# Performance work log

Measured on AMD Instinct MI355X. Metric: run time of the kernel, lower is better.

Reference implementation:

```python
import jax, jax.numpy as jnp
import numpy as np

N, E, IN, H, OUT, K = 50000, 800000, 128, 64, 64, 1024


def setup_inputs() -> dict:
    key = jax.random.key(0)
    ks = jax.random.split(key, 8)
    x = jax.random.normal(ks[0], (N, IN), dtype=jnp.float32)
    edge_index = jax.random.randint(ks[1], (2, E), 0, N, dtype=jnp.int32)
    cluster_id = jax.random.randint(ks[2], (N,), 0, K, dtype=jnp.int32)
    W1 = jax.random.normal(ks[3], (IN, H), dtype=jnp.float32) / np.float32(np.sqrt(IN))
    b1 = jnp.zeros((H,), jnp.float32)
    W2 = jax.random.normal(ks[4], (H, OUT), dtype=jnp.float32) / np.float32(np.sqrt(H))
    b2 = jnp.zeros((OUT,), jnp.float32)
    W_skip = jax.random.normal(ks[5], (H, OUT), dtype=jnp.float32) / np.float32(np.sqrt(H))
    b_skip = jnp.zeros((OUT,), jnp.float32)
    alpha = jnp.full((1,), 1.5, jnp.float32)
    return dict(x=x, edge_index=edge_index, cluster_id=cluster_id, W1=W1, b1=b1,
                W2=W2, b2=b2, W_skip=W_skip, b_skip=b_skip, alpha=alpha)


def gcn_conv_sparse(x, src, dst, n, W, b):
    # PyG GCNConv: transform, then D^{-1/2}(A+I)D^{-1/2} aggregation, then bias.
    h = x @ W  # [n, F_out]
    deg = jax.ops.segment_sum(jnp.ones_like(src, dtype=h.dtype), dst, num_segments=n) + 1.0
    dinv = jax.lax.rsqrt(deg)
    norm = dinv[src] * dinv[dst]  # [E]
    agg = jax.ops.segment_sum(h[src] * norm[:, None], dst, num_segments=n)
    agg = agg + (dinv * dinv)[:, None] * h  # self-loop term
    return agg + b


def reference(x, edge_index, cluster_id, W1, b1, W2, b2, W_skip, b_skip, alpha):
    src, dst = edge_index[0], edge_index[1]
    # conv1 + ReLU (dropout is identity in eval mode)
    x1 = jax.nn.relu(gcn_conv_sparse(x, src, dst, N, W1, b1))  # [N, H]

    # pool_by_partition: scatter-mean node features into K clusters
    sums = jax.ops.segment_sum(x1, cluster_id, num_segments=K)  # [K, H]
    counts = jnp.maximum(jax.ops.segment_sum(jnp.ones((N,), x1.dtype), cluster_id, num_segments=K), 1.0)
    x_p = sums / counts[:, None]

    # deduped pooled edges, self-loops removed == dense 0/1 adjacency with zero diag (K small)
    cu, cv = cluster_id[src], cluster_id[dst]
    A = jnp.zeros((K, K), x1.dtype).at[cu, cv].set(1.0)
    A = A * (1.0 - jnp.eye(K, dtype=x1.dtype))
    A_hat = A + jnp.eye(K, dtype=x1.dtype)
    deg_p = jnp.sum(A_hat, axis=0)  # in-degree at target (PyG computes deg on col)
    dinv_p = jax.lax.rsqrt(deg_p)
    A_norm = dinv_p[:, None] * A_hat * dinv_p[None, :]  # [src, dst]
    h_p = x_p @ W2
    x_p2 = jnp.einsum('st,sf->tf', A_norm, h_p) + b2  # [K, OUT]

    # gather-broadcast + strengthened skip head
    up = x_p2[cluster_id]  # [N, OUT]
    skip = x1 @ W_skip + b_skip
    logits = up + jax.nn.relu(alpha)[0] * skip
    return logits
```

## Files before the change

kernel.cpp:

```cpp
#include <hip/hip_runtime.h>
#include <hip/hip_fp16.h>

#define NN 50000
#define NE 800000
#define FIN 128
#define FH 64
#define FOUT 64
#define KC 1024
#define CAP 64
#define EPB 2048
#define NCH ((NE + EPB - 1) / EPB)
#define NBK ((NN + 255) / 256)
#define BCAP 4608

typedef unsigned char  u8;
typedef unsigned short u16;
typedef unsigned int   u32;

__global__ __launch_bounds__(256) void k_part(const int* __restrict__ src,
                                              const int* __restrict__ dst,
                                              const int* __restrict__ cid,
                                              int* __restrict__ gcur,
                                              u32* __restrict__ bin,
                                              u8* __restrict__ AT) {
    __shared__ int hist[256], off[256], cur[256], gbase[256];
    __shared__ u32 raw[EPB];
    __shared__ u32 sorted[EPB];
    int t = threadIdx.x;
    hist[t] = 0; cur[t] = 0;
    __syncthreads();
    int e0 = blockIdx.x * EPB, e1 = min(NE, e0 + EPB);
    int cnt = e1 - e0;
    for (int e = e0 + t; e < e1; e += 256) {
        int d = dst[e], s = src[e];
        int b = d >> 8, local = d & 255;
        int cu = cid[s], cv = cid[d];
        if (cu != cv) AT[(size_t)cv * KC + cu] = 1;
        atomicAdd(&hist[b], 1);
        raw[e - e0] = ((u32)b << 24) | ((u32)local << 16) | (u32)s;
    }
    __syncthreads();
    int v = hist[t];
    off[t] = v;
    __syncthreads();
    for (int o = 1; o < 256; o <<= 1) {
        int u = (t >= o) ? off[t - o] : 0;
        __syncthreads();
        off[t] += u;
        __syncthreads();
    }
    int ex = off[t] - v;
    __syncthreads();
    off[t] = ex;
    __syncthreads();
    for (int i = t; i < cnt; i += 256) {
        u32 e = raw[i];
        int b = e >> 24;
        int p = off[b] + atomicAdd(&cur[b], 1);
        sorted[p] = e;
    }
    __syncthreads();
    if (t < NBK && hist[t]) gbase[t] = atomicAdd(&gcur[t], hist[t]);
    __syncthreads();
    for (int i = t; i < cnt; i += 256) {
        u32 e = sorted[i];
        int b = e >> 24;
        int idx = gbase[b] + (i - off[b]);
        if (idx < BCAP) bin[(size_t)b * BCAP + idx] = e;
    }
}

__global__ __launch_bounds__(256) void k_slots(const int* __restrict__ gcur,
                                               const u32* __restrict__ bin,
                                               const int* __restrict__ cid,
                                               int* __restrict__ deg,
                                               float* __restrict__ dinv,
                                               int* __restrict__ counts,
                                               u16* __restrict__ slots) {
    __shared__ u16 sbuf[256 * CAP];
    __shared__ int c_lds[256];
    int t = threadIdx.x, b = blockIdx.x;
    c_lds[t] = 0;
    __syncthreads();
    int cnt = min(gcur[b], BCAP);
    const u32* bp = bin + (size_t)b * BCAP;
    for (int i = t; i < cnt; i += 256) {
        u32 e = bp[i];
        int local = (e >> 16) & 255;
        int pos = atomicAdd(&c_lds[local], 1);
        if (pos < CAP) sbuf[local * CAP + pos] = (u16)(e & 0xffffu);
    }
    __syncthreads();
    int node = b * 256 + t;
    if (node < NN) {
        int d = c_lds[t];
        deg[node] = d;
        dinv[node] = rsqrtf((float)d + 1.0f);
        atomicAdd(&counts[cid[node]], 1);
    }
    int rows = min(256, NN - b * 256);
    int n4 = rows * (CAP * 2 / 16);
    const uint4* sb4 = (const uint4*)sbuf;
    uint4* gs4 = (uint4*)(slots + (size_t)b * 256 * CAP);
    for (int j = t; j < n4; j += 256) gs4[j] = sb4[j];
}

__global__ __launch_bounds__(256) void k_gemm1(const float* __restrict__ x,
                                               const float* __restrict__ W1,
                                               const float* __restrict__ dinv,
                                               __half* __restrict__ h) {
    __shared__ float Ws[FIN * FH];
    __shared__ float Xs[32 * FIN];
    int t = threadIdx.x;
    int row_base = blockIdx.x * 32;
    for (int i = t; i < FIN * FH; i += 256) Ws[i] = W1[i];
    {
        const float4* x4 = (const float4*)x;
        float4* xs4 = (float4*)Xs;
        for (int i = t; i < 32 * 32; i += 256) {
            int r = i >> 5, k4 = i & 31;
            int row = row_base + r;
            float4 v = make_float4(0.f, 0.f, 0.f, 0.f);
            if (row < NN) v = x4[(size_t)row * 32 + k4];
            xs4[i] = v;
        }
    }
    __syncthreads();
    int c = t & 31, grp = t >> 5;
    int colp = c * 2;
    int r0 = grp * 4;
    const float4* p0 = (const float4*)&Xs[(r0 + 0) * FIN];
    const float4* p1 = (const float4*)&Xs[(r0 + 1) * FIN];
    const float4* p2 = (const float4*)&Xs[(r0 + 2) * FIN];
    const float4* p3 = (const float4*)&Xs[(r0 + 3) * FIN];
    float acc00 = 0.f, acc01 = 0.f, acc10 = 0.f, acc11 = 0.f;
    float acc20 = 0.f, acc21 = 0.f, acc30 = 0.f, acc31 = 0.f;
#pragma unroll 2
    for (int k4 = 0; k4 < FIN / 4; ++k4) {
        float4 a0 = p0[k4], a1 = p1[k4], a2 = p2[k4], a3 = p3[k4];
        const float* wb = &Ws[(k4 * 4) * FH + colp];
        float2 w0 = *(const float2*)&wb[0];
        float2 w1 = *(const float2*)&wb[FH];
        float2 w2 = *(const float2*)&wb[2 * FH];
        float2 w3 = *(const float2*)&wb[3 * FH];
        acc00 = fmaf(a0.x, w0.x, fmaf(a0.y, w1.x, fmaf(a0.z, w2.x, fmaf(a0.w, w3.x, acc00))));
        acc01 = fmaf(a0.x, w0.y, fmaf(a0.y, w1.y, fmaf(a0.z, w2.y, fmaf(a0.w, w3.y, acc01))));
        acc10 = fmaf(a1.x, w0.x, fmaf(a1.y, w1.x, fmaf(a1.z, w2.x, fmaf(a1.w, w3.x, acc10))));
        acc11 = fmaf(a1.x, w0.y, fmaf(a1.y, w1.y, fmaf(a1.z, w2.y, fmaf(a1.w, w3.y, acc11))));
        acc20 = fmaf(a2.x, w0.x, fmaf(a2.y, w1.x, fmaf(a2.z, w2.x, fmaf(a2.w, w3.x, acc20))));
        acc21 = fmaf(a2.x, w0.y, fmaf(a2.y, w1.y, fmaf(a2.z, w2.y, fmaf(a2.w, w3.y, acc21))));
        acc30 = fmaf(a3.x, w0.x, fmaf(a3.y, w1.x, fmaf(a3.z, w2.x, fmaf(a3.w, w3.x, acc30))));
        acc31 = fmaf(a3.x, w0.y, fmaf(a3.y, w1.y, fmaf(a3.z, w2.y, fmaf(a3.w, w3.y, acc31))));
    }
    __half2* h2 = (__half2*)h;
    int row0 = row_base + r0;
    if (row0 + 0 < NN) { float di = dinv[row0 + 0]; h2[(size_t)(row0 + 0) * 32 + c] = __floats2half2_rn(di * acc00, di * acc01); }
    if (row0 + 1 < NN) { float di = dinv[row0 + 1]; h2[(size_t)(row0 + 1) * 32 + c] = __floats2half2_rn(di * acc10, di * acc11); }
    if (row0 + 2 < NN) { float di = dinv[row0 + 2]; h2[(size_t)(row0 + 2) * 32 + c] = __floats2half2_rn(di * acc20, di * acc21); }
    if (row0 + 3 < NN) { float di = dinv[row0 + 3]; h2[(size_t)(row0 + 3) * 32 + c] = __floats2half2_rn(di * acc30, di * acc31); }
}

__global__ __launch_bounds__(256) void k_gather(const int* __restrict__ deg,
                                                const u16* __restrict__ slots,
                                                const float* __restrict__ dinv,
                                                const __half* __restrict__ h,
                                                const float* __restrict__ b1,
                                                const int* __restrict__ cid,
                                                __half* __restrict__ x1,
                                                float* __restrict__ sums) {
    int lane = threadIdx.x & 63;
    int node = blockIdx.x * 4 + (threadIdx.x >> 6);
    if (node >= NN) return;
    int g = lane >> 3, w = lane & 7;
    const uint4* h16 = (const uint4*)h;
    int cnt = min(deg[node], CAP);
    const u16* cp = slots + (size_t)node * CAP;
    float a0 = 0.f, a1 = 0.f, a2 = 0.f, a3 = 0.f;
    float a4 = 0.f, a5 = 0.f, a6 = 0.f, a7 = 0.f;
    int s = (lane < cnt) ? (int)cp[lane] : 0;
    int nFull = cnt >> 3;
    for (int j = 0; j < nFull; ++j) {
        int ss = __shfl(s, j * 8 + g);
        uint4 u = h16[(size_t)ss * 8 + w];
        float2 f0 = __half22float2(*(__half2*)&u.x);
        float2 f1 = __half22float2(*(__half2*)&u.y);
        float2 f2 = __half22float2(*(__half2*)&u.z);
        float2 f3 = __half22float2(*(__half2*)&u.w);
        a0 += f0.x; a1 += f0.y; a2 += f1.x; a3 += f1.y;
        a4 += f2.x; a5 += f2.y; a6 += f3.x; a7 += f3.y;
    }
    int tail = cnt & 7;
    if (tail) {
        int ss = __shfl(s, nFull * 8 + g);
        float m = (g < tail) ? 1.f : 0.f;
        uint4 u = h16[(size_t)ss * 8 + w];
        float2 f0 = __half22float2(*(__half2*)&u.x);
        float2 f1 = __half22float2(*(__half2*)&u.y);
        float2 f2 = __half22float2(*(__half2*)&u.z);
        float2 f3 = __half22float2(*(__half2*)&u.w);
        a0 = fmaf(m, f0.x, a0); a1 = fmaf(m, f0.y, a1);
        a2 = fmaf(m, f1.x, a2); a3 = fmaf(m, f1.y, a3);
        a4 = fmaf(m, f2.x, a4); a5 = fmaf(m, f2.y, a5);
        a6 = fmaf(m, f3.x, a6); a7 = fmaf(m, f3.y, a7);
    }
#pragma unroll
    for (int msk = 8; msk <= 32; msk <<= 1) {
        a0 += __shfl_xor(a0, msk); a1 += __shfl_xor(a1, msk);
        a2 += __shfl_xor(a2, msk); a3 += __shfl_xor(a3, msk);
        a4 += __shfl_xor(a4, msk); a5 += __shfl_xor(a5, msk);
        a6 += __shfl_xor(a6, msk); a7 += __shfl_xor(a7, msk);
    }
    float di = dinv[node];
    uint4 su = h16[(size_t)node * 8 + w];
    float2 s0 = __half22float2(*(__half2*)&su.x);
    float2 s1 = __half22float2(*(__half2*)&su.y);
    float2 s2 = __half22float2(*(__half2*)&su.z);
    float2 s3 = __half22float2(*(__half2*)&su.w);
    const float4* b14 = (const float4*)b1;
    float4 bA = b14[w * 2], bB = b14[w * 2 + 1];
    float v0 = fmaxf(fmaf(di, a0 + s0.x, bA.x), 0.f);
    float v1 = fmaxf(fmaf(di, a1 + s0.y, bA.y), 0.f);
    float v2 = fmaxf(fmaf(di, a2 + s1.x, bA.z), 0.f);
    float v3 = fmaxf(fmaf(di, a3 + s1.y, bA.w), 0.f);
    float v4 = fmaxf(fmaf(di, a4 + s2.x, bB.x), 0.f);
    float v5 = fmaxf(fmaf(di, a5 + s2.y, bB.y), 0.f);
    float v6 = fmaxf(fmaf(di, a6 + s3.x, bB.z), 0.f);
    float v7 = fmaxf(fmaf(di, a7 + s3.y, bB.w), 0.f);
    if (g == 0) {
        __half2 q0 = __floats2half2_rn(v0, v1);
        __half2 q1 = __floats2half2_rn(v2, v3);
        __half2 q2 = __floats2half2_rn(v4, v5);
        __half2 q3 = __floats2half2_rn(v6, v7);
        uint4 ou;
        ou.x = *(u32*)&q0; ou.y = *(u32*)&q1; ou.z = *(u32*)&q2; ou.w = *(u32*)&q3;
        ((uint4*)x1)[(size_t)node * 8 + w] = ou;
    }
    float mine = (g == 0) ? v0 : (g == 1) ? v1 : (g == 2) ? v2 : (g == 3) ? v3
               : (g == 4) ? v4 : (g == 5) ? v5 : (g == 6) ? v6 : v7;
    int c = cid[node];
    unsafeAtomicAdd(&sums[(size_t)c * FH + w * 8 + g], mine);
}

__global__ __launch_bounds__(64) void k_pool(const float* __restrict__ sums,
                                             const int* __restrict__ counts,
                                             const float* __restrict__ W2,
                                             const u8* __restrict__ AT,
                                             float* __restrict__ dinvp,
                                             float* __restrict__ g) {
    __shared__ float xp[FH];
    int s = blockIdx.x, f = threadIdx.x;
    const u32* row = (const u32*)(AT + (size_t)s * KC);
    int pc = __popc(row[f]) + __popc(row[f + 64]) + __popc(row[f + 128]) + __popc(row[f + 192]);
    for (int o = 32; o; o >>= 1) pc += __shfl_xor(pc, o);
    float dp = rsqrtf(1.0f + (float)pc);
    if (f == 0) dinvp[s] = dp;
    float cnt = fmaxf((float)counts[s], 1.0f);
    xp[f] = sums[(size_t)s * FH + f] / cnt;
    __syncthreads();
    float acc = 0.f;
    for (int j = 0; j < FH; ++j) acc = fmaf(xp[j], W2[j * FH + f], acc);
    g[(size_t)s * FH + f] = dp * acc;
}

__global__ __launch_bounds__(256) void k_xp2(const u8* __restrict__ AT,
                                             const float* __restrict__ g,
                                             const float* __restrict__ dinvp,
                                             const float* __restrict__ b2,
                                             float* __restrict__ xp2) {
    __shared__ float4 sm4[4][16];
    int t = blockIdx.x;
    int lane = threadIdx.x & 63, w = threadIdx.x >> 6;
    int q = lane >> 4, fl = lane & 15;
    const u32* roww = (const u32*)(AT + (size_t)t * KC);
    const float4* g4 = (const float4*)g;
    float4 acc = make_float4(0.f, 0.f, 0.f, 0.f);
    int wb = w * 64;
    u32 wv = roww[wb + lane];
    for (int j = 0; j < 16; ++j) {
        u32 word = __shfl((int)wv, j * 4 + q);
        int sidx = (wb + j * 4 + q) * 4;
#pragma unroll
        for (int b = 0; b < 4; ++b) {
            float a = (float)((word >> (8 * b)) & 255u);
            float4 gv = g4[(size_t)(sidx + b) * 16 + fl];
            acc.x = fmaf(a, gv.x, acc.x);
            acc.y = fmaf(a, gv.y, acc.y);
            acc.z = fmaf(a, gv.z, acc.z);
            acc.w = fmaf(a, gv.w, acc.w);
        }
    }
    acc.x += __shfl_xor(acc.x, 16); acc.y += __shfl_xor(acc.y, 16);
    acc.z += __shfl_xor(acc.z, 16); acc.w += __shfl_xor(acc.w, 16);
    acc.x += __shfl_xor(acc.x, 32); acc.y += __shfl_xor(acc.y, 32);
    acc.z += __shfl_xor(acc.z, 32); acc.w += __shfl_xor(acc.w, 32);
    if (q == 0) sm4[w][fl] = acc;
    __syncthreads();
    if (threadIdx.x < 16) {
        int f = threadIdx.x;
        float4 a0 = sm4[0][f], a1 = sm4[1][f], a2 = sm4[2][f], a3 = sm4[3][f];
        float4 gs = g4[(size_t)t * 16 + f];
        float dp = dinvp[t];
        const float4* b24 = (const float4*)b2;
        float4 bb = b24[f];
        float4 o;
        o.x = fmaf(dp, a0.x + a1.x + a2.x + a3.x + gs.x, bb.x);
        o.y = fmaf(dp, a0.y + a1.y + a2.y + a3.y + gs.y, bb.y);
        o.z = fmaf(dp, a0.z + a1.z + a2.z + a3.z + gs.z, bb.z);
        o.w = fmaf(dp, a0.w + a1.w + a2.w + a3.w + gs.w, bb.w);
        ((float4*)xp2)[(size_t)t * 16 + f] = o;
    }
}

__global__ __launch_bounds__(256) void k_final(const __half* __restrict__ x1,
                                               const float* __restrict__ Wsk,
                                               const float* __restrict__ bsk,
                                               const float* __restrict__ xp2,
                                               const int* __restrict__ cid,
                                               const float* __restrict__ alpha,
                                               float* __restrict__ out) {
    __shared__ float Ws[FH * FOUT];
    __shared__ float Xs[32 * FH];
    int t = threadIdx.x;
    int row_base = blockIdx.x * 32;
    for (int i = t; i < FH * FOUT; i += 256) Ws[i] = Wsk[i];
    {
        const uint4* x16 = (const uint4*)x1;
        int r = t >> 3, k8 = t & 7;
        int row = row_base + r;
        uint4 u = make_uint4(0u, 0u, 0u, 0u);
        if (row < NN) u = x16[(size_t)row * 8 + k8];
        float2 f0 = __half22float2(*(__half2*)&u.x);
        float2 f1 = __half22float2(*(__half2*)&u.y);
        float2 f2 = __half22float2(*(__half2*)&u.z);
        float2 f3 = __half22float2(*(__half2*)&u.w);
        float4* dstp = (float4*)&Xs[r * FH + k8 * 8];
        dstp[0] = make_float4(f0.x, f0.y, f1.x, f1.y);
        dstp[1] = make_float4(f2.x, f2.y, f3.x, f3.y);
    }
    __syncthreads();
    float al = fmaxf(alpha[0], 0.f);
    int col = t & 31, grp = t >> 5;
    int r0 = grp * 4;
    const float4* p0 = (const float4*)&Xs[(r0 + 0) * FH];
    const float4* p1 = (const float4*)&Xs[(r0 + 1) * FH];
    const float4* p2 = (const float4*)&Xs[(r0 + 2) * FH];
    const float4* p3 = (const float4*)&Xs[(r0 + 3) * FH];
    float acc00 = 0.f, acc01 = 0.f, acc10 = 0.f, acc11 = 0.f;
    float acc20 = 0.f, acc21 = 0.f, acc30 = 0.f, acc31 = 0.f;
#pragma unroll 2
    for (int k4 = 0; k4 < FH / 4; ++k4) {
        float4 a0 = p0[k4], a1 = p1[k4], a2 = p2[k4], a3 = p3[k4];
        const float* wp = &Ws[(k4 * 4) * FOUT + col];
        float w00 = wp[0],           w01 = wp[32];
        float w10 = wp[FOUT],        w11 = wp[FOUT + 32];
        float w20 = wp[2 * FOUT],    w21 = wp[2 * FOUT + 32];
        float w30 = wp[3 * FOUT],    w31 = wp[3 * FOUT + 32];
        acc00 = fmaf(a0.x, w00, fmaf(a0.y, w10, fmaf(a0.z, w20, fmaf(a0.w, w30, acc00))));
        acc01 = fmaf(a0.x, w01, fmaf(a0.y, w11, fmaf(a0.z, w21, fmaf(a0.w, w31, acc01))));
        acc10 = fmaf(a1.x, w00, fmaf(a1.y, w10, fmaf(a1.z, w20, fmaf(a1.w, w30, acc10))));
        acc11 = fmaf(a1.x, w01, fmaf(a1.y, w11, fmaf(a1.z, w21, fmaf(a1.w, w31, acc11))));
        acc20 = fmaf(a2.x, w00, fmaf(a2.y, w10, fmaf(a2.z, w20, fmaf(a2.w, w30, acc20))));
        acc21 = fmaf(a2.x, w01, fmaf(a2.y, w11, fmaf(a2.z, w21, fmaf(a2.w, w31, acc21))));
        acc30 = fmaf(a3.x, w00, fmaf(a3.y, w10, fmaf(a3.z, w20, fmaf(a3.w, w30, acc30))));
        acc31 = fmaf(a3.x, w01, fmaf(a3.y, w11, fmaf(a3.z, w21, fmaf(a3.w, w31, acc31))));
    }
    float bb0 = bsk[col], bb1 = bsk[col + 32];
    int row0 = row_base + r0;
#pragma unroll
    for (int i = 0; i < 4; ++i) {
        float a0 = (i == 0) ? acc00 : (i == 1) ? acc10 : (i == 2) ? acc20 : acc30;
        float a1 = (i == 0) ? acc01 : (i == 1) ? acc11 : (i == 2) ? acc21 : acc31;
        int row = row0 + i;
        if (row < NN) {
            int c = cid[row];
            out[(size_t)row * FOUT + col]      = xp2[(size_t)c * FOUT + col]      + al * (a0 + bb0);
            out[(size_t)row * FOUT + col + 32] = xp2[(size_t)c * FOUT + col + 32] + al * (a1 + bb1);
        }
    }
}

extern "C" void kernel_launch(void* const* d_in, const int* in_sizes, int n_in,
                              void* d_out, int out_size, void* d_ws, size_t ws_size,
                              hipStream_t stream) {
    const float* x    = (const float*)d_in[0];
    const int*   ei   = (const int*)d_in[1];
    const int*   cid  = (const int*)d_in[2];
    const float* W1   = (const float*)d_in[3];
    const float* b1   = (const float*)d_in[4];
    const float* W2   = (const float*)d_in[5];
    const float* b2   = (const float*)d_in[6];
    const float* Wsk  = (const float*)d_in[7];
    const float* bsk  = (const float*)d_in[8];
    const float* alpha= (const float*)d_in[9];
    float* out = (float*)d_out;
    const int* src = ei;
    const int* dst = ei + NE;

    char* ws = (char*)d_ws;
    size_t cur = 0;
    auto alloc = [&](size_t nb) { cur = (cur + 255) & ~(size_t)255; size_t o = cur; cur += nb; return o; };
    size_t o_sums = alloc((size_t)KC * FH * 4);
    size_t o_AT   = alloc((size_t)KC * KC);
    size_t o_cnt  = alloc((size_t)KC * 4);
    size_t o_gcur = alloc((size_t)NBK * 4);
    size_t zero_bytes = cur;
    size_t o_bin  = alloc((size_t)NBK * BCAP * 4);
    size_t o_slot = alloc((size_t)NN * CAP * 2);
    size_t o_deg  = alloc((size_t)NN * 4);
    size_t o_x1   = alloc((size_t)NN * FH * 2);
    size_t o_h    = alloc((size_t)NN * FH * 2);
    size_t o_dinv = alloc((size_t)NN * 4);
    size_t o_g    = alloc((size_t)KC * FH * 4);
    size_t o_xp2  = alloc((size_t)KC * FH * 4);
    size_t o_dinvp= alloc((size_t)KC * 4);
    (void)ws_size; (void)in_sizes; (void)n_in; (void)out_size;

    float* sums = (float*)(ws + o_sums);
    u8*    AT   = (u8*)(ws + o_AT);
    int*   cnt  = (int*)(ws + o_cnt);
    int*   gcur = (int*)(ws + o_gcur);
    u32*   bin  = (u32*)(ws + o_bin);
    u16*   slot = (u16*)(ws + o_slot);
    int*   deg  = (int*)(ws + o_deg);
    __half* x1  = (__half*)(ws + o_x1);
    __half* h   = (__half*)(ws + o_h);
    float* dinv = (float*)(ws + o_dinv);
    float* g    = (float*)(ws + o_g);
    float* xp2  = (float*)(ws + o_xp2);
    float* dinvp= (float*)(ws + o_dinvp);

    hipMemsetAsync(d_ws, 0, zero_bytes, stream);

    const int NRB = (NN + 31) / 32;
    k_part  <<<NCH, 256, 0, stream>>>(src, dst, cid, gcur, bin, AT);
    k_slots <<<NBK, 256, 0, stream>>>(gcur, bin, cid, deg, dinv, cnt, slot);
    k_gemm1 <<<NRB, 256, 0, stream>>>(x, W1, dinv, h);
    k_gather<<<(NN + 3) / 4, 256, 0, stream>>>(deg, slot, dinv, h, b1, cid, x1, sums);
    k_pool  <<<KC, 64, 0, stream>>>(sums, cnt, W2, AT, dinvp, g);
    k_xp2   <<<KC, 256, 0, stream>>>(AT, g, dinvp, b2, xp2);
    k_final <<<NRB, 256, 0, stream>>>(x1, Wsk, bsk, xp2, cid, alpha, out);
}
```

Before: 202.7 us.

## Compute degree in partition pass and merge slot build with first GEMM

Node in-degrees are now accumulated with global atomics during the edge partition pass, so the first GEMM no longer depends on the slot-building kernel. The slot-building and GEMM kernels are then merged into one launch whose blocks branch on their index, which removes a launch and lets the two independent workloads run concurrently. The GEMM epilogue computes dinv from the degree itself and writes it out. The cost is 800k extra global atomics in the partition pass and a 48KB shared allocation for every block, which may limit occupancy. Degrees are also no longer capped by the bin capacity.

```diff
diff --git a/kernel.cpp b/kernel.cpp
--- a/kernel.cpp
+++ b/kernel.cpp
@@ -12,6 +12,7 @@
 #define NCH ((NE + EPB - 1) / EPB)
 #define NBK ((NN + 255) / 256)
 #define BCAP 4608
+#define NRB ((NN + 31) / 32)
 
 typedef unsigned char  u8;
 typedef unsigned short u16;
@@ -20,6 +21,7 @@
 __global__ __launch_bounds__(256) void k_part(const int* __restrict__ src,
                                               const int* __restrict__ dst,
                                               const int* __restrict__ cid,
+                                              int* __restrict__ deg,
                                               int* __restrict__ gcur,
                                               u32* __restrict__ bin,
                                               u8* __restrict__ AT) {
@@ -36,6 +38,7 @@
         int b = d >> 8, local = d & 255;
         int cu = cid[s], cv = cid[d];
         if (cu != cv) AT[(size_t)cv * KC + cu] = 1;
+        atomicAdd(&deg[d], 1);
         atomicAdd(&hist[b], 1);
         raw[e - e0] = ((u32)b << 24) | ((u32)local << 16) | (u32)s;
     }
@@ -70,49 +73,45 @@
     }
 }
 
-__global__ __launch_bounds__(256) void k_slots(const int* __restrict__ gcur,
-                                               const u32* __restrict__ bin,
-                                               const int* __restrict__ cid,
-                                               int* __restrict__ deg,
-                                               float* __restrict__ dinv,
-                                               int* __restrict__ counts,
-                                               u16* __restrict__ slots) {
-    __shared__ u16 sbuf[256 * CAP];
-    __shared__ int c_lds[256];
-    int t = threadIdx.x, b = blockIdx.x;
-    c_lds[t] = 0;
-    __syncthreads();
-    int cnt = min(gcur[b], BCAP);
-    const u32* bp = bin + (size_t)b * BCAP;
-    for (int i = t; i < cnt; i += 256) {
-        u32 e = bp[i];
-        int local = (e >> 16) & 255;
-        int pos = atomicAdd(&c_lds[local], 1);
-        if (pos < CAP) sbuf[local * CAP + pos] = (u16)(e & 0xffffu);
-    }
-    __syncthreads();
-    int node = b * 256 + t;
-    if (node < NN) {
-        int d = c_lds[t];
-        deg[node] = d;
-        dinv[node] = rsqrtf((float)d + 1.0f);
-        atomicAdd(&counts[cid[node]], 1);
-    }
-    int rows = min(256, NN - b * 256);
-    int n4 = rows * (CAP * 2 / 16);
-    const uint4* sb4 = (const uint4*)sbuf;
-    uint4* gs4 = (uint4*)(slots + (size_t)b * 256 * CAP);
-    for (int j = t; j < n4; j += 256) gs4[j] = sb4[j];
-}
-
-__global__ __launch_bounds__(256) void k_gemm1(const float* __restrict__ x,
-                                               const float* __restrict__ W1,
-                                               const float* __restrict__ dinv,
-                                               __half* __restrict__ h) {
-    __shared__ float Ws[FIN * FH];
-    __shared__ float Xs[32 * FIN];
+__global__ __launch_bounds__(256) void k_prep(const int* __restrict__ gcur,
+                                              const u32* __restrict__ bin,
+                                              const int* __restrict__ cid,
+                                              const int* __restrict__ deg,
+                                              float* __restrict__ dinv,
+                                              int* __restrict__ counts,
+                                              u16* __restrict__ slots,
+                                              const float* __restrict__ x,
+                                              const float* __restrict__ W1,
+                                              __half* __restrict__ h) {
+    __shared__ __align__(16) char smem[49152];
     int t = threadIdx.x;
-    int row_base = blockIdx.x * 32;
+    if (blockIdx.x < NBK) {
+        u16* sbuf  = (u16*)smem;
+        int* c_lds = (int*)(smem + 32768);
+        int b = blockIdx.x;
+        c_lds[t] = 0;
+        __syncthreads();
+        int cnt = min(gcur[b], BCAP);
+        const u32* bp = bin + (size_t)b * BCAP;
+        for (int i = t; i < cnt; i += 256) {
+            u32 e = bp[i];
+            int local = (e >> 16) & 255;
+            int pos = atomicAdd(&c_lds[local], 1);
+            if (pos < CAP) sbuf[local * CAP + pos] = (u16)(e & 0xffffu);
+        }
+        __syncthreads();
+        int node = b * 256 + t;
+        if (node < NN) atomicAdd(&counts[cid[node]], 1);
+        int rows = min(256, NN - b * 256);
+        int n4 = rows * (CAP * 2 / 16);
+        const uint4* sb4 = (const uint4*)sbuf;
+        uint4* gs4 = (uint4*)(slots + (size_t)b * 256 * CAP);
+        for (int j = t; j < n4; j += 256) gs4[j] = sb4[j];
+        return;
+    }
+    float* Ws = (float*)smem;
+    float* Xs = (float*)(smem + 32768);
+    int row_base = (blockIdx.x - NBK) * 32;
     for (int i = t; i < FIN * FH; i += 256) Ws[i] = W1[i];
     {
         const float4* x4 = (const float4*)x;
@@ -154,10 +153,17 @@
     }
     __half2* h2 = (__half2*)h;
     int row0 = row_base + r0;
-    if (row0 + 0 < NN) { float di = dinv[row0 + 0]; h2[(size_t)(row0 + 0) * 32 + c] = __floats2half2_rn(di * acc00, di * acc01); }
-    if (row0 + 1 < NN) { float di = dinv[row0 + 1]; h2[(size_t)(row0 + 1) * 32 + c] = __floats2half2_rn(di * acc10, di * acc11); }
-    if (row0 + 2 < NN) { float di = dinv[row0 + 2]; h2[(size_t)(row0 + 2) * 32 + c] = __floats2half2_rn(di * acc20, di * acc21); }
-    if (row0 + 3 < NN) { float di = dinv[row0 + 3]; h2[(size_t)(row0 + 3) * 32 + c] = __floats2half2_rn(di * acc30, di * acc31); }
+#pragma unroll
+    for (int i = 0; i < 4; ++i) {
+        int row = row0 + i;
+        if (row < NN) {
+            float di = rsqrtf((float)deg[row] + 1.0f);
+            if (c == 0) dinv[row] = di;
+            float aa = (i == 0) ? acc00 : (i == 1) ? acc10 : (i == 2) ? acc20 : acc30;
+            float ab = (i == 0) ? acc01 : (i == 1) ? acc11 : (i == 2) ? acc21 : acc31;
+            h2[(size_t)row * 32 + c] = __floats2half2_rn(di * aa, di * ab);
+        }
+    }
 }
 
 __global__ __launch_bounds__(256) void k_gather(const int* __restrict__ deg,
@@ -403,10 +409,10 @@
     size_t o_AT   = alloc((size_t)KC * KC);
     size_t o_cnt  = alloc((size_t)KC * 4);
     size_t o_gcur = alloc((size_t)NBK * 4);
+    size_t o_deg  = alloc((size_t)NN * 4);
     size_t zero_bytes = cur;
     size_t o_bin  = alloc((size_t)NBK * BCAP * 4);
     size_t o_slot = alloc((size_t)NN * CAP * 2);
-    size_t o_deg  = alloc((size_t)NN * 4);
     size_t o_x1   = alloc((size_t)NN * FH * 2);
     size_t o_h    = alloc((size_t)NN * FH * 2);
     size_t o_dinv = alloc((size_t)NN * 4);
@@ -419,9 +425,9 @@
     u8*    AT   = (u8*)(ws + o_AT);
     int*   cnt  = (int*)(ws + o_cnt);
     int*   gcur = (int*)(ws + o_gcur);
+    int*   deg  = (int*)(ws + o_deg);
     u32*   bin  = (u32*)(ws + o_bin);
     u16*   slot = (u16*)(ws + o_slot);
-    int*   deg  = (int*)(ws + o_deg);
     __half* x1  = (__half*)(ws + o_x1);
     __half* h   = (__half*)(ws + o_h);
     float* dinv = (float*)(ws + o_dinv);
@@ -431,10 +437,8 @@
 
     hipMemsetAsync(d_ws, 0, zero_bytes, stream);
 
-    const int NRB = (NN + 31) / 32;
-    k_part  <<<NCH, 256, 0, stream>>>(src, dst, cid, gcur, bin, AT);
-    k_slots <<<NBK, 256, 0, stream>>>(gcur, bin, cid, deg, dinv, cnt, slot);
-    k_gemm1 <<<NRB, 256, 0, stream>>>(x, W1, dinv, h);
+    k_part  <<<NCH, 256, 0, stream>>>(src, dst, cid, deg, gcur, bin, AT);
+    k_prep  <<<NBK + NRB, 256, 0, stream>>>(gcur, bin, cid, deg, dinv, cnt, slot, x, W1, h);
     k_gather<<<(NN + 3) / 4, 256, 0, stream>>>(deg, slot, dinv, h, b1, cid, x1, sums);
     k_pool  <<<KC, 64, 0, stream>>>(sums, cnt, W2, AT, dinvp, g);
     k_xp2   <<<KC, 256, 0, stream>>>(AT, g, dinvp, b2, xp2);
```

Result: slower. 221.0 us (+9.0%).

## Replace atomic cluster-sum scatter with per-cluster node lists gathered in pool

Applied to the files above, without the earlier changes.

The float atomic scatter of x1 into per-cluster sums inside the gather kernel is removed. k_slots now builds a capped per-cluster node list, and k_pool reads and averages x1 rows for each cluster directly. Separately, the edges handled per block in the partition kernel are halved. The change trades 3.2M contended atomics for a serial per-cluster gather loop in k_pool, and it truncates clusters larger than 128 nodes, which risks wrong results if a cluster overflows.

```diff
diff --git a/kernel.cpp b/kernel.cpp
--- a/kernel.cpp
+++ b/kernel.cpp
@@ -8,10 +8,11 @@
 #define FOUT 64
 #define KC 1024
 #define CAP 64
-#define EPB 2048
+#define EPB 1024
 #define NCH ((NE + EPB - 1) / EPB)
 #define NBK ((NN + 255) / 256)
 #define BCAP 4608
+#define CCAP 128
 
 typedef unsigned char  u8;
 typedef unsigned short u16;
@@ -75,7 +76,8 @@
                                                const int* __restrict__ cid,
                                                int* __restrict__ deg,
                                                float* __restrict__ dinv,
-                                               int* __restrict__ counts,
+                                               int* __restrict__ clcur,
+                                               u16* __restrict__ clist,
                                                u16* __restrict__ slots) {
     __shared__ u16 sbuf[256 * CAP];
     __shared__ int c_lds[256];
@@ -96,7 +98,9 @@
         int d = c_lds[t];
         deg[node] = d;
         dinv[node] = rsqrtf((float)d + 1.0f);
-        atomicAdd(&counts[cid[node]], 1);
+        int c = cid[node];
+        int pos = atomicAdd(&clcur[c], 1);
+        if (pos < CCAP) clist[(size_t)c * CCAP + pos] = (u16)node;
     }
     int rows = min(256, NN - b * 256);
     int n4 = rows * (CAP * 2 / 16);
@@ -165,9 +169,7 @@
                                                 const float* __restrict__ dinv,
                                                 const __half* __restrict__ h,
                                                 const float* __restrict__ b1,
-                                                const int* __restrict__ cid,
-                                                __half* __restrict__ x1,
-                                                float* __restrict__ sums) {
+                                                __half* __restrict__ x1) {
     int lane = threadIdx.x & 63;
     int node = blockIdx.x * 4 + (threadIdx.x >> 6);
     if (node >= NN) return;
@@ -210,23 +212,23 @@
         a4 += __shfl_xor(a4, msk); a5 += __shfl_xor(a5, msk);
         a6 += __shfl_xor(a6, msk); a7 += __shfl_xor(a7, msk);
     }
-    float di = dinv[node];
-    uint4 su = h16[(size_t)node * 8 + w];
-    float2 s0 = __half22float2(*(__half2*)&su.x);
-    float2 s1 = __half22float2(*(__half2*)&su.y);
-    float2 s2 = __half22float2(*(__half2*)&su.z);
-    float2 s3 = __half22float2(*(__half2*)&su.w);
-    const float4* b14 = (const float4*)b1;
-    float4 bA = b14[w * 2], bB = b14[w * 2 + 1];
-    float v0 = fmaxf(fmaf(di, a0 + s0.x, bA.x), 0.f);
-    float v1 = fmaxf(fmaf(di, a1 + s0.y, bA.y), 0.f);
-    float v2 = fmaxf(fmaf(di, a2 + s1.x, bA.z), 0.f);
-    float v3 = fmaxf(fmaf(di, a3 + s1.y, bA.w), 0.f);
-    float v4 = fmaxf(fmaf(di, a4 + s2.x, bB.x), 0.f);
-    float v5 = fmaxf(fmaf(di, a5 + s2.y, bB.y), 0.f);
-    float v6 = fmaxf(fmaf(di, a6 + s3.x, bB.z), 0.f);
-    float v7 = fmaxf(fmaf(di, a7 + s3.y, bB.w), 0.f);
     if (g == 0) {
+        float di = dinv[node];
+        uint4 su = h16[(size_t)node * 8 + w];
+        float2 s0 = __half22float2(*(__half2*)&su.x);
+        float2 s1 = __half22float2(*(__half2*)&su.y);
+        float2 s2 = __half22float2(*(__half2*)&su.z);
+        float2 s3 = __half22float2(*(__half2*)&su.w);
+        const float4* b14 = (const float4*)b1;
+        float4 bA = b14[w * 2], bB = b14[w * 2 + 1];
+        float v0 = fmaxf(fmaf(di, a0 + s0.x, bA.x), 0.f);
+        float v1 = fmaxf(fmaf(di, a1 + s0.y, bA.y), 0.f);
+        float v2 = fmaxf(fmaf(di, a2 + s1.x, bA.z), 0.f);
+        float v3 = fmaxf(fmaf(di, a3 + s1.y, bA.w), 0.f);
+        float v4 = fmaxf(fmaf(di, a4 + s2.x, bB.x), 0.f);
+        float v5 = fmaxf(fmaf(di, a5 + s2.y, bB.y), 0.f);
+        float v6 = fmaxf(fmaf(di, a6 + s3.x, bB.z), 0.f);
+        float v7 = fmaxf(fmaf(di, a7 + s3.y, bB.w), 0.f);
         __half2 q0 = __floats2half2_rn(v0, v1);
         __half2 q1 = __floats2half2_rn(v2, v3);
         __half2 q2 = __floats2half2_rn(v4, v5);
@@ -235,14 +237,11 @@
         ou.x = *(u32*)&q0; ou.y = *(u32*)&q1; ou.z = *(u32*)&q2; ou.w = *(u32*)&q3;
         ((uint4*)x1)[(size_t)node * 8 + w] = ou;
     }
-    float mine = (g == 0) ? v0 : (g == 1) ? v1 : (g == 2) ? v2 : (g == 3) ? v3
-               : (g == 4) ? v4 : (g == 5) ? v5 : (g == 6) ? v6 : v7;
-    int c = cid[node];
-    unsafeAtomicAdd(&sums[(size_t)c * FH + w * 8 + g], mine);
-}
-
-__global__ __launch_bounds__(64) void k_pool(const float* __restrict__ sums,
-                                             const int* __restrict__ counts,
+}
+
+__global__ __launch_bounds__(64) void k_pool(const u16* __restrict__ clist,
+                                             const int* __restrict__ clcur,
+                                             const __half* __restrict__ x1,
                                              const float* __restrict__ W2,
                                              const u8* __restrict__ AT,
                                              float* __restrict__ dinvp,
@@ -254,12 +253,18 @@
     for (int o = 32; o; o >>= 1) pc += __shfl_xor(pc, o);
     float dp = rsqrtf(1.0f + (float)pc);
     if (f == 0) dinvp[s] = dp;
-    float cnt = fmaxf((float)counts[s], 1.0f);
-    xp[f] = sums[(size_t)s * FH + f] / cnt;
-    __syncthreads();
+    int cnt = min(clcur[s], CCAP);
+    const u16* np = clist + (size_t)s * CCAP;
     float acc = 0.f;
-    for (int j = 0; j < FH; ++j) acc = fmaf(xp[j], W2[j * FH + f], acc);
-    g[(size_t)s * FH + f] = dp * acc;
+    for (int i = 0; i < cnt; ++i) {
+        int node = np[i];
+        acc += __half2float(x1[(size_t)node * FH + f]);
+    }
+    xp[f] = acc / fmaxf((float)cnt, 1.0f);
+    __syncthreads();
+    float a2 = 0.f;
+    for (int j = 0; j < FH; ++j) a2 = fmaf(xp[j], W2[j * FH + f], a2);
+    g[(size_t)s * FH + f] = dp * a2;
 }
 
 __global__ __launch_bounds__(256) void k_xp2(const u8* __restrict__ AT,
@@ -399,13 +404,13 @@
     char* ws = (char*)d_ws;
     size_t cur = 0;
     auto alloc = [&](size_t nb) { cur = (cur + 255) & ~(size_t)255; size_t o = cur; cur += nb; return o; };
-    size_t o_sums = alloc((size_t)KC * FH * 4);
     size_t o_AT   = alloc((size_t)KC * KC);
-    size_t o_cnt  = alloc((size_t)KC * 4);
     size_t o_gcur = alloc((size_t)NBK * 4);
+    size_t o_clc  = alloc((size_t)KC * 4);
     size_t zero_bytes = cur;
     size_t o_bin  = alloc((size_t)NBK * BCAP * 4);
     size_t o_slot = alloc((size_t)NN * CAP * 2);
+    size_t o_clist= alloc((size_t)KC * CCAP * 2);
     size_t o_deg  = alloc((size_t)NN * 4);
     size_t o_x1   = alloc((size_t)NN * FH * 2);
     size_t o_h    = alloc((size_t)NN * FH * 2);
@@ -415,12 +420,12 @@
     size_t o_dinvp= alloc((size_t)KC * 4);
     (void)ws_size; (void)in_sizes; (void)n_in; (void)out_size;
 
-    float* sums = (float*)(ws + o_sums);
     u8*    AT   = (u8*)(ws + o_AT);
-    int*   cnt  = (int*)(ws + o_cnt);
     int*   gcur = (int*)(ws + o_gcur);
+    int*   clc  = (int*)(ws + o_clc);
     u32*   bin  = (u32*)(ws + o_bin);
     u16*   slot = (u16*)(ws + o_slot);
+    u16*   clist= (u16*)(ws + o_clist);
     int*   deg  = (int*)(ws + o_deg);
     __half* x1  = (__half*)(ws + o_x1);
     __half* h   = (__half*)(ws + o_h);
@@ -433,10 +438,10 @@
 
     const int NRB = (NN + 31) / 32;
     k_part  <<<NCH, 256, 0, stream>>>(src, dst, cid, gcur, bin, AT);
-    k_slots <<<NBK, 256, 0, stream>>>(gcur, bin, cid, deg, dinv, cnt, slot);
+    k_slots <<<NBK, 256, 0, stream>>>(gcur, bin, cid, deg, dinv, clc, clist, slot);
     k_gemm1 <<<NRB, 256, 0, stream>>>(x, W1, dinv, h);
-    k_gather<<<(NN + 3) / 4, 256, 0, stream>>>(deg, slot, dinv, h, b1, cid, x1, sums);
-    k_pool  <<<KC, 64, 0, stream>>>(sums, cnt, W2, AT, dinvp, g);
+    k_gather<<<(NN + 3) / 4, 256, 0, stream>>>(deg, slot, dinv, h, b1, x1);
+    k_pool  <<<KC, 64, 0, stream>>>(clist, clc, x1, W2, AT, dinvp, g);
     k_xp2   <<<KC, 256, 0, stream>>>(AT, g, dinvp, b2, xp2);
     k_final <<<NRB, 256, 0, stream>>>(x1, Wsk, bsk, xp2, cid, alpha, out);
 }
```

Measured after the change: 238.9 us. 17.8% more time.
